# Kernel optimization log

Hardware: AMD Instinct MI355X
Metric: run time of the kernel (lower is better)

## Reference

```python
import jax, jax.numpy as jnp
import numpy as np

N, E, D, STEPS, MOLS, OUT = 50000, 400000, 128, 3, 256, 32


def setup_inputs() -> dict:
    key = jax.random.key(0)
    ks = jax.random.split(key, 20)
    s = 0.1  # weight scale ~ 1/sqrt(fan_in) to keep relu chain stable
    inp = {
        "states": jax.random.normal(ks[0], (N, D), jnp.float32),
        "Win": jax.random.normal(ks[1], (STEPS, 2 * D, 64), jnp.float32) * s,
        "b_in": jax.random.normal(ks[2], (STEPS, 64), jnp.float32) * s,
        "Wh": jax.random.normal(ks[3], (STEPS, 64, 64), jnp.float32) * s,
        "b_h": jax.random.normal(ks[4], (STEPS, 64), jnp.float32) * s,
        "Wout": jax.random.normal(ks[5], (STEPS, 64, D), jnp.float32) * s,
        "b_out": jax.random.normal(ks[6], (STEPS, D), jnp.float32) * s,
        "fc1_w": jax.random.normal(ks[7], (D, 64), jnp.float32) * s,
        "fc1_b": jax.random.normal(ks[8], (64,), jnp.float32) * s,
        "fc2_w": jax.random.normal(ks[9], (64, 64), jnp.float32) * s,
        "fc2_b": jax.random.normal(ks[10], (64,), jnp.float32) * s,
        "out_w": jax.random.normal(ks[11], (64, OUT), jnp.float32) * s,
        "out_b": jax.random.normal(ks[12], (OUT,), jnp.float32) * s,
        "src": jax.random.randint(ks[13], (E,), 0, N, jnp.int32).astype(jnp.int64),
        "dst": jax.random.randint(ks[14], (E,), 0, N, jnp.int32).astype(jnp.int64),
        "mol_ids": jax.random.randint(ks[15], (N,), 0, MOLS, jnp.int32).astype(jnp.int64),
        "num_mols": MOLS,
    }
    return inp


def reference(states, Win, b_in, Wh, b_h, Wout, b_out,
              fc1_w, fc1_b, fc2_w, fc2_b, out_w, out_b,
              src, dst, mol_ids, num_mols):
    n_atoms = states.shape[0]
    s = states
    for t in range(Win.shape[0]):  # message_steps (small, static)
        # per-edge message input: concat(owner state, neighbor state) -> [E, 2D]
        x = jnp.concatenate([s[dst], s[src]], axis=-1)
        m = jax.nn.relu(x @ Win[t] + b_in[t])
        m = jax.nn.relu(m @ Wh[t] + b_h[t])
        m = jax.nn.relu(m @ Wout[t] + b_out[t])  # [E, D]
        # atom-wise sum aggregation of incoming messages
        s = jax.ops.segment_sum(m, dst, num_segments=n_atoms)
    # molecule representation: sum of final atom states per molecule
    mol_repr = jax.ops.segment_sum(s, mol_ids, num_segments=num_mols)  # [M, D]
    h = jax.nn.relu(mol_repr @ fc1_w + fc1_b)
    h = jax.nn.relu(h @ fc2_w + fc2_b)
    return h @ out_w + out_b  # [M, OUT]
```

## Files before the change

kernel.cpp:

```cpp
#include <hip/hip_runtime.h>

typedef unsigned long long u64;
typedef unsigned short ushort_t;

#define NA 50000
#define NE 400000
#define DF 128
#define HID 64
#define NMOL 256
#define NOUT 32
#define NSTEP 3
#define NPB 782

#define RNG 8192
#define NRNG 7
#define NCH 64
#define CHUNK 6250
#define NCHM 16
#define CHM 3125
#define NWB 336
#define HISTB (NRNG*NCH + NCHM + NWB)
#define SCATB (NRNG*NCH + NCHM)
#define MBUF_ROWS 160000

typedef __attribute__((ext_vector_type(8))) unsigned short ushort8;
typedef __attribute__((ext_vector_type(4))) float f32x4;
typedef __attribute__((ext_vector_type(8))) _Float16 half8;
typedef __attribute__((ext_vector_type(2))) _Float16 half2_t;
typedef __attribute__((ext_vector_type(2))) __fp16 fp16x2;

static __device__ __forceinline__ ushort_t f2h(float f) {
  union { _Float16 h; ushort_t u; } v; v.h = (_Float16)f; return v.u;
}
static __device__ __forceinline__ float hlo(unsigned d) {
  union { unsigned u; half2_t h; } v; v.u = d; return (float)v.h[0];
}
static __device__ __forceinline__ float hhi(unsigned d) {
  union { unsigned u; half2_t h; } v; v.u = d; return (float)v.h[1];
}
static __device__ __forceinline__ unsigned pkrtz(float a, float b) {
  union { fp16x2 h; unsigned u; } v;
  v.h = __builtin_amdgcn_cvt_pkrtz(a, b);
  return v.u;
}

__global__ __launch_bounds__(256) void hist_all(
    const int* __restrict__ dst, const int* __restrict__ mol_ids,
    const float* __restrict__ Win, const float* __restrict__ Wh,
    const float* __restrict__ Wout,
    ushort_t* __restrict__ WpB, ushort_t* __restrict__ WhB,
    ushort_t* __restrict__ WoB,
    ushort_t* __restrict__ H, unsigned* __restrict__ MH,
    int* __restrict__ mcnt) {
  __shared__ unsigned hist[RNG];
  const int b = blockIdx.x, t = threadIdx.x;
  if (b < NRNG * NCH) {
    const int r = b / NCH, c = b % NCH;
    const int lo = r * RNG;
    for (int i = t; i < RNG; i += 256) hist[i] = 0;
    __syncthreads();
    const int base = c * CHUNK;
    for (int k = t; k < CHUNK; k += 256) {
      int d = dst[base + k];
      unsigned rel = (unsigned)(d - lo);
      if (rel < RNG) atomicAdd(&hist[rel], 1u);
    }
    __syncthreads();
    ushort_t* Hp = H + (u64)b * RNG;
    for (int i = t; i < RNG; i += 256) Hp[i] = (ushort_t)hist[i];
    return;
  }
  int b2 = b - NRNG * NCH;
  if (b2 < NCHM) {
    if (t < 256) hist[t] = 0;
    __syncthreads();
    const int base = b2 * CHM;
    for (int k = t; k < CHM; k += 256) atomicAdd(&hist[mol_ids[base + k]], 1u);
    __syncthreads();
    if (t < 256) {
      MH[b2 * 256 + t] = hist[t];
      if (hist[t]) atomicAdd(&mcnt[t], (int)hist[t]);
    }
    return;
  }
  int g = (b2 - NCHM) * 256 + t;
  if (g < 3 * 16384) {
    int tt = g / 16384, r = g % 16384;
    int j = r & 7, lane = (r >> 3) & 63, f = r >> 9;
    int kc = f & 3, nt = f >> 2;
    int k = kc * 32 + (lane >> 4) * 8 + j;
    int n = nt * 16 + (lane & 15);
    float v = (n < 64) ? Win[tt * 16384 + k * 64 + n]
                       : Win[tt * 16384 + (128 + k) * 64 + (n - 64)];
    WpB[g] = f2h(v);
  }
  int g2 = g - 3 * 16384;
  if (g2 >= 0 && g2 < 3 * 4096) {
    int tt = g2 / 4096, r = g2 % 4096;
    int j = r & 7, lane = (r >> 3) & 63, f = r >> 9;
    int kc = f & 1, nt = f >> 1;
    int k = kc * 32 + (lane >> 4) * 8 + j;
    int n = nt * 16 + (lane & 15);
    WhB[g2] = f2h(Wh[tt * 4096 + k * 64 + n]);
  }
  int g3 = g2 - 3 * 4096;
  if (g3 >= 0 && g3 < 3 * 8192) {
    int tt = g3 / 8192, r = g3 % 8192;
    int j = r & 7, lane = (r >> 3) & 63, f = r >> 9;
    int kc = f & 1, nt = f >> 1;
    int k = kc * 32 + (lane >> 4) * 8 + j;
    int n = nt * 16 + (lane & 15);
    WoB[g3] = f2h(Wout[tt * 8192 + k * 128 + n]);
  }
}

__global__ void col_scan(const ushort_t* __restrict__ H,
                         ushort_t* __restrict__ Orel, int* __restrict__ counts) {
  int bidx = blockIdx.x * 256 + threadIdx.x;
  if (bidx >= NA) return;
  int r = bidx >> 13, i = bidx & (RNG - 1);
  const ushort_t* Hp = H + ((u64)r * NCH) * RNG + i;
  unsigned acc = 0;
  for (int c = 0; c < NCH; c++) {
    Orel[(u64)c * NA + bidx] = (ushort_t)acc;
    acc += Hp[(u64)c * RNG];
  }
  counts[bidx] = (int)acc;
}

__global__ void scan_phase1(const int* __restrict__ counts, int* __restrict__ tmp,
                            int* __restrict__ blk,
                            const int* __restrict__ mcnt, int* __restrict__ mrow) {
  __shared__ int sh[1024];
  int t = threadIdx.x;
  int i = blockIdx.x * 1024 + t;
  sh[t] = (i < NA) ? counts[i] : 0;
  __syncthreads();
  for (int off = 1; off < 1024; off <<= 1) {
    int x = (t >= off) ? sh[t - off] : 0;
    __syncthreads();
    sh[t] += x;
    __syncthreads();
  }
  if (i < NA) tmp[i] = sh[t];
  if (t == 1023) blk[blockIdx.x] = sh[1023];
  if (blockIdx.x == gridDim.x - 1) {
    __syncthreads();
    sh[t] = (t < NMOL) ? mcnt[t] : 0;
    __syncthreads();
    for (int off = 1; off < NMOL; off <<= 1) {
      int x = (t >= off && t < NMOL) ? sh[t - off] : 0;
      __syncthreads();
      if (t < NMOL) sh[t] += x;
      __syncthreads();
    }
    if (t < NMOL) mrow[t + 1] = sh[t];
    if (t == 0) mrow[0] = 0;
  }
}

__global__ void scan_phase3(const int* __restrict__ tmp, const int* __restrict__ blk,
                            int* __restrict__ row_ptr,
                            int* __restrict__ ntmp, int* __restrict__ nblk) {
  __shared__ int sh[1024];
  __shared__ int spre_sh;
  int t = threadIdx.x;
  int bid = blockIdx.x;
  if (t < 64) {
    int v = (t < bid) ? blk[t] : 0;
    for (int off = 32; off; off >>= 1) v += __shfl_down(v, off);
    if (t == 0) spre_sh = v;
  }
  __syncthreads();
  int spre = spre_sh;
  int i = bid * 1024 + t;
  int nwin = 0;
  if (i < NA) {
    int re = tmp[i] + spre;
    int rs = (t == 0) ? spre : (tmp[i - 1] + spre);
    row_ptr[i + 1] = re;
    if (re > rs) nwin = ((re - 1) >> 2) - (rs >> 2) + 1;
  }
  if (i == 0) row_ptr[0] = 0;
  sh[t] = nwin;
  __syncthreads();
  for (int off = 1; off < 1024; off <<= 1) {
    int x = (t >= off) ? sh[t - off] : 0;
    __syncthreads();
    sh[t] += x;
    __syncthreads();
  }
  if (i < NA) ntmp[i] = sh[t];
  if (t == 1023) nblk[bid] = sh[1023];
}

__global__ void nscan_p3(const int* __restrict__ ntmp, const int* __restrict__ nblk,
                         const int* __restrict__ row_ptr,
                         int* __restrict__ orow, int* __restrict__ orow2) {
  __shared__ int spre_sh;
  int t = threadIdx.x;
  int bid = blockIdx.x;
  if (t < 64) {
    int v = (t < bid) ? nblk[t] : 0;
    for (int off = 32; off; off >>= 1) v += __shfl_down(v, off);
    if (t == 0) spre_sh = v;
  }
  __syncthreads();
  int spre = spre_sh;
  int i = bid * 1024 + t;
  if (i < NA) {
    orow[i + 1] = ntmp[i] + spre;
    int oi = (t == 0) ? spre : (ntmp[i - 1] + spre);
    orow2[i] = oi - (row_ptr[i] >> 2);
  }
  if (i == 0) orow[0] = 0;
}

__global__ __launch_bounds__(256) void scat_all(
    const int* __restrict__ dst, const int* __restrict__ src,
    const int* __restrict__ row_ptr, const ushort_t* __restrict__ Orel,
    unsigned* __restrict__ ds_pack,
    const int* __restrict__ mol_ids, const int* __restrict__ mrow,
    const unsigned* __restrict__ MH, int* __restrict__ mol_sorted) {
  __shared__ unsigned cnt[RNG];
  __shared__ unsigned mbase[256];
  const int b = blockIdx.x, t = threadIdx.x;
  if (b < NRNG * NCH) {
    const int r = b / NCH, c = b % NCH;
    const int lo = r * RNG;
    for (int i = t; i < RNG; i += 256) cnt[i] = 0;
    __syncthreads();
    const int base = c * CHUNK;
    const ushort_t* Op = Orel + (u64)c * NA;
    for (int k = t; k < CHUNK; k += 256) {
      int e = base + k;
      int d = dst[e];
      unsigned rel = (unsigned)(d - lo);
      if (rel < RNG) {
        unsigned lr = atomicAdd(&cnt[rel], 1u);
        int pos = row_ptr[d] + (int)Op[d] + (int)lr;
        ds_pack[pos] = ((unsigned)d << 16) | (unsigned)src[e];
      }
    }
    return;
  }
  const int c2 = b - NRNG * NCH;
  if (t < 256) {
    unsigned s = (unsigned)mrow[t];
    for (int cp = 0; cp < c2; cp++) s += MH[cp * 256 + t];
    mbase[t] = s;
    cnt[t] = 0;
  }
  __syncthreads();
  const int base = c2 * CHM;
  for (int k = t; k < CHM; k += 256) {
    int a = base + k;
    int m = mol_ids[a];
    unsigned lr = atomicAdd(&cnt[m], 1u);
    mol_sorted[mbase[m] + lr] = a;
  }
}

__global__ __launch_bounds__(256) void node_proj(
    const float* __restrict__ s_in, const ushort_t* __restrict__ WpB,
    const float* __restrict__ b_in, ushort_t* __restrict__ PQb) {
  const int t = threadIdx.x;
  const int lane = t & 63, wv = t >> 6, quad = lane >> 4, l15 = lane & 15;
  const int n0 = blockIdx.x * 64 + wv * 16;
  int n = n0 + l15; if (n >= NA) n = NA - 1;
  union { half8 v; unsigned d[4]; } a[4];
#pragma unroll
  for (int c = 0; c < 4; c++) {
    const float* p = s_in + (u64)n * 128 + c * 32 + quad * 8;
    float4 f0 = *(const float4*)(p);
    float4 f1 = *(const float4*)(p + 4);
    a[c].d[0] = pkrtz(f0.x, f0.y);
    a[c].d[1] = pkrtz(f0.z, f0.w);
    a[c].d[2] = pkrtz(f1.x, f1.y);
    a[c].d[3] = pkrtz(f1.z, f1.w);
  }
  float binv[4];
#pragma unroll
  for (int nt = 0; nt < 4; nt++) binv[nt] = b_in[nt * 16 + l15];
#pragma unroll
  for (int nt = 0; nt < 8; nt++) {
    f32x4 acc = {0.f, 0.f, 0.f, 0.f};
#pragma unroll
    for (int c = 0; c < 4; c++) {
      half8 b = *(const half8*)&WpB[((nt * 4 + c) * 64 + lane) * 8];
      acc = __builtin_amdgcn_mfma_f32_16x16x32_f16(a[c].v, b, acc, 0, 0, 0);
    }
    float bias = (nt < 4) ? binv[nt] : 0.f;
#pragma unroll
    for (int r = 0; r < 4; r++) {
      int nn = n0 + quad * 4 + r;
      if (nn < NA) PQb[(u64)nn * 128 + nt * 16 + l15] = f2h(acc[r] + bias);
    }
  }
}

__global__ __launch_bounds__(256) void edge_msg(
    const ushort_t* __restrict__ PQb,
    const ushort_t* __restrict__ WhB, const ushort_t* __restrict__ WoB,
    const float* __restrict__ b_h, const float* __restrict__ b_out,
    const unsigned* __restrict__ ds_pack, const int* __restrict__ orow2,
    unsigned* __restrict__ m_buf) {
  __shared__ unsigned eps[128];
  __shared__ int ops[128];
  __shared__ ushort_t h2s[4][16 * 72];
  const int t = threadIdx.x;
  const int lane = t & 63, wv = t >> 6, quad = lane >> 4, l15 = lane & 15;
  const long long e0 = (long long)blockIdx.x * 128;

  if (t < 128) {
    long long e = e0 + t;
    unsigned pk = ds_pack[e];
    eps[t] = pk;
    ops[t] = orow2[pk >> 16] + (int)(e >> 2);
  }
  float bh[4], bo[8];
#pragma unroll
  for (int nt = 0; nt < 4; nt++) bh[nt] = b_h[nt * 16 + l15];
#pragma unroll
  for (int nt = 0; nt < 8; nt++) bo[nt] = b_out[nt * 16 + l15];
  __syncthreads();

  union PQ { ushort8 v; half2_t h[4]; } pv[2][2], qv[2][2];
#pragma unroll
  for (int i = 0; i < 2; i++) {
    unsigned pk = eps[wv * 32 + i * 16 + l15];
    int da = pk >> 16, sa = pk & 0xffffu;
#pragma unroll
    for (int c = 0; c < 2; c++) {
      const int col = c * 32 + quad * 8;
      pv[i][c].v = *(const ushort8*)&PQb[(u64)da * 128 + col];
      qv[i][c].v = *(const ushort8*)&PQb[(u64)sa * 128 + 64 + col];
    }
  }

  const half2_t z2 = {(_Float16)0.f, (_Float16)0.f};
#pragma unroll
  for (int i = 0; i < 2; i++) {
    const int ebl = wv * 32 + i * 16;

    union { half8 v; half2_t h[4]; } a1[2];
#pragma unroll
    for (int c = 0; c < 2; c++) {
#pragma unroll
      for (int k = 0; k < 4; k++) {
        half2_t s = pv[i][c].h[k] + qv[i][c].h[k];
        a1[c].h[k] = __builtin_elementwise_max(s, z2);
      }
    }

    ushort_t* hb = h2s[wv];
#pragma unroll
    for (int nt = 0; nt < 4; nt++) {
      f32x4 acc = {0.f, 0.f, 0.f, 0.f};
#pragma unroll
      for (int c = 0; c < 2; c++) {
        half8 b = *(const half8*)&WhB[((nt * 2 + c) * 64 + lane) * 8];
        acc = __builtin_amdgcn_mfma_f32_16x16x32_f16(a1[c].v, b, acc, 0, 0, 0);
      }
#pragma unroll
      for (int r = 0; r < 4; r++)
        hb[(quad * 4 + r) * 72 + nt * 16 + l15] =
            f2h(fmaxf(acc[r] + bh[nt], 0.f));
    }

    half8 a2[2];
#pragma unroll
    for (int c = 0; c < 2; c++)
      a2[c] = *(const half8*)&hb[l15 * 72 + c * 32 + quad * 8];

    f32x4 acc2[8];
#pragma unroll
    for (int nt = 0; nt < 8; nt++) {
      f32x4 acc = {0.f, 0.f, 0.f, 0.f};
#pragma unroll
      for (int c = 0; c < 2; c++) {
        half8 b = *(const half8*)&WoB[((nt * 2 + c) * 64 + lane) * 8];
        acc = __builtin_amdgcn_mfma_f32_16x16x32_f16(a2[c], b, acc, 0, 0, 0);
      }
      acc2[nt] = acc;
    }

    {
      const int base = ebl + quad * 4;
      int prev = (int)(eps[base] >> 16);
      int orow_ = ops[base];
      float run[8];
#pragma unroll
      for (int nt = 0; nt < 8; nt++) run[nt] = 0.f;
#pragma unroll
      for (int r = 0; r < 4; r++) {
        int er = base + r;
        int dcur = (int)(eps[er] >> 16);
        if (dcur != prev) {
          unsigned* rowp = m_buf + (u64)orow_ * 64;
#pragma unroll
          for (int k = 0; k < 4; k++)
            rowp[k * 16 + l15] = pkrtz(run[2 * k], run[2 * k + 1]);
#pragma unroll
          for (int nt = 0; nt < 8; nt++) run[nt] = 0.f;
          prev = dcur; orow_ = ops[er];
        }
#pragma unroll
        for (int nt = 0; nt < 8; nt++)
          run[nt] += fmaxf(acc2[nt][r] + bo[nt], 0.f);
      }
      unsigned* rowp = m_buf + (u64)orow_ * 64;
#pragma unroll
      for (int k = 0; k < 4; k++)
        rowp[k * 16 + l15] = pkrtz(run[2 * k], run[2 * k + 1]);
    }
  }
}

__global__ __launch_bounds__(256) void agg_proj(
    const unsigned* __restrict__ m_buf, const int* __restrict__ orow,
    const ushort_t* __restrict__ WpB, const float* __restrict__ b_in,
    ushort_t* __restrict__ PQb) {
  __shared__ ushort_t a_s[64 * 136];
  __shared__ int obs_s[65];
  const int t = threadIdx.x;
  const int lane = t & 63, wv = t >> 6, quad = lane >> 4, l15 = lane & 15;
  const int n0 = blockIdx.x * 64;
  if (t < 65) {
    int idx = n0 + t; if (idx > NA) idx = NA;
    obs_s[t] = orow[idx];
  }
  __syncthreads();

  for (int r = 0; r < 16; r++) {
    const int d = n0 + wv * 16 + r;
    float s0 = 0.f, s1 = 0.f;
    if (d < NA) {
      int ob = obs_s[wv * 16 + r], oe = obs_s[wv * 16 + r + 1];
      int n = oe - ob;
      float t0 = 0.f, t1 = 0.f, u0 = 0.f, u1 = 0.f, v0 = 0.f, v1 = 0.f;
      int full = n & ~3;
      int e = ob;
      for (; e < ob + full; e += 4) {
        unsigned w0 = m_buf[(u64)(e + 0) * 64 + lane];
        unsigned w1 = m_buf[(u64)(e + 1) * 64 + lane];
        unsigned w2 = m_buf[(u64)(e + 2) * 64 + lane];
        unsigned w3 = m_buf[(u64)(e + 3) * 64 + lane];
        s0 += hlo(w0); s1 += hhi(w0);
        t0 += hlo(w1); t1 += hhi(w1);
        u0 += hlo(w2); u1 += hhi(w2);
        v0 += hlo(w3); v1 += hhi(w3);
      }
      int rem = n - full;
      if (rem > 0) {
        int i1 = (rem > 1) ? e + 1 : e;
        int i2 = (rem > 2) ? e + 2 : e;
        unsigned w0 = m_buf[(u64)e * 64 + lane];
        unsigned w1 = m_buf[(u64)i1 * 64 + lane];
        unsigned w2 = m_buf[(u64)i2 * 64 + lane];
        s0 += hlo(w0); s1 += hhi(w0);
        if (rem > 1) { t0 += hlo(w1); t1 += hhi(w1); }
        if (rem > 2) { u0 += hlo(w2); u1 += hhi(w2); }
      }
      s0 = (s0 + t0) + (u0 + v0);
      s1 = (s1 + t1) + (u1 + v1);
    }
    const int row = wv * 16 + r;
    a_s[row * 136 + quad * 32 + l15] = f2h(s0);
    a_s[row * 136 + quad * 32 + 16 + l15] = f2h(s1);
  }

  float binv[4];
#pragma unroll
  for (int nt = 0; nt < 4; nt++) binv[nt] = b_in[nt * 16 + l15];
  half8 a[4];
#pragma unroll
  for (int c = 0; c < 4; c++)
    a[c] = *(const half8*)&a_s[(wv * 16 + l15) * 136 + c * 32 + quad * 8];
#pragma unroll
  for (int nt = 0; nt < 8; nt++) {
    f32x4 acc = {0.f, 0.f, 0.f, 0.f};
#pragma unroll
    for (int c = 0; c < 4; c++) {
      half8 b = *(const half8*)&WpB[((nt * 4 + c) * 64 + lane) * 8];
      acc = __builtin_amdgcn_mfma_f32_16x16x32_f16(a[c], b, acc, 0, 0, 0);
    }
    float bias = (nt < 4) ? binv[nt] : 0.f;
#pragma unroll
    for (int r = 0; r < 4; r++) {
      int nn = n0 + wv * 16 + quad * 4 + r;
      if (nn < NA) PQb[(u64)nn * 128 + nt * 16 + l15] = f2h(acc[r] + bias);
    }
  }
}

__global__ __launch_bounds__(256) void agg_mol2(
    const unsigned* __restrict__ m_buf, const int* __restrict__ orow,
    const int* __restrict__ mol_sorted, const int* __restrict__ mol_ids,
    float* __restrict__ mol_repr) {
  __shared__ int mids[64], obs[64], oes[64];
  const int t = threadIdx.x;
  const int lane = t & 63, wv = t >> 6;
  const int base = blockIdx.x * 64;
  if (t < 64) {
    int idx = base + t;
    int r = (idx < NA) ? mol_sorted[idx] : 0;
    mids[t] = (idx < NA) ? mol_ids[r] : -1;
    obs[t] = orow[r];
    oes[t] = orow[r + 1];
  }
  __syncthreads();
  const int c0 = (lane >> 4) * 32 + (lane & 15);
  float r0 = 0.f, r1 = 0.f;
  int prev = mids[wv * 16];
  for (int i = 0; i < 16; i++) {
    int li = wv * 16 + i;
    int m = mids[li];
    if (m != prev) {
      if (prev >= 0) {
        atomicAdd(&mol_repr[(u64)prev * 128 + c0], r0);
        atomicAdd(&mol_repr[(u64)prev * 128 + c0 + 16], r1);
      }
      r0 = 0.f; r1 = 0.f; prev = m;
    }
    if (m >= 0) {
      int ob = obs[li], oe = oes[li];
      int n = oe - ob;
      float t0 = 0.f, t1 = 0.f, u0 = 0.f, u1 = 0.f, v0 = 0.f, v1 = 0.f;
      int full = n & ~3;
      int e = ob;
      for (; e < ob + full; e += 4) {
        unsigned w0 = m_buf[(u64)(e + 0) * 64 + lane];
        unsigned w1 = m_buf[(u64)(e + 1) * 64 + lane];
        unsigned w2 = m_buf[(u64)(e + 2) * 64 + lane];
        unsigned w3 = m_buf[(u64)(e + 3) * 64 + lane];
        r0 += hlo(w0); r1 += hhi(w0);
        t0 += hlo(w1); t1 += hhi(w1);
        u0 += hlo(w2); u1 += hhi(w2);
        v0 += hlo(w3); v1 += hhi(w3);
      }
      int rem = n - full;
      if (rem > 0) {
        int i1 = (rem > 1) ? e + 1 : e;
        int i2 = (rem > 2) ? e + 2 : e;
        unsigned w0 = m_buf[(u64)e * 64 + lane];
        unsigned w1 = m_buf[(u64)i1 * 64 + lane];
        unsigned w2 = m_buf[(u64)i2 * 64 + lane];
        r0 += hlo(w0); r1 += hhi(w0);
        if (rem > 1) { t0 += hlo(w1); t1 += hhi(w1); }
        if (rem > 2) { u0 += hlo(w2); u1 += hhi(w2); }
      }
      r0 += (t0 + u0) + v0;
      r1 += (t1 + u1) + v1;
    }
  }
  if (prev >= 0) {
    atomicAdd(&mol_repr[(u64)prev * 128 + c0], r0);
    atomicAdd(&mol_repr[(u64)prev * 128 + c0 + 16], r1);
  }
}

__global__ void final_mlp(const float* __restrict__ mol_repr,
                          const float* __restrict__ fc1_w, const float* __restrict__ fc1_b,
                          const float* __restrict__ fc2_w, const float* __restrict__ fc2_b,
                          const float* __restrict__ out_w, const float* __restrict__ out_b,
                          float* __restrict__ out) {
  int m = blockIdx.x, j = threadIdx.x;
  __shared__ float h1sh[64], h2sh[64];
  const float* mr = mol_repr + (u64)m * DF;
  float acc = fc1_b[j];
  for (int d = 0; d < DF; d++) acc = fmaf(mr[d], fc1_w[d * 64 + j], acc);
  h1sh[j] = fmaxf(acc, 0.f);
  __syncthreads();
  acc = fc2_b[j];
  for (int k = 0; k < 64; k++) acc = fmaf(h1sh[k], fc2_w[k * 64 + j], acc);
  h2sh[j] = fmaxf(acc, 0.f);
  __syncthreads();
  if (j < NOUT) {
    acc = out_b[j];
    for (int k = 0; k < 64; k++) acc = fmaf(h2sh[k], out_w[k * NOUT + j], acc);
    out[(u64)m * NOUT + j] = acc;
  }
}

extern "C" void kernel_launch(void* const* d_in, const int* in_sizes, int n_in,
                              void* d_out, int out_size, void* d_ws, size_t ws_size,
                              hipStream_t stream) {
  const float* states = (const float*)d_in[0];
  const float* Win    = (const float*)d_in[1];
  const float* b_in   = (const float*)d_in[2];
  const float* Wh     = (const float*)d_in[3];
  const float* b_h    = (const float*)d_in[4];
  const float* Wout   = (const float*)d_in[5];
  const float* b_out  = (const float*)d_in[6];
  const float* fc1_w  = (const float*)d_in[7];
  const float* fc1_b  = (const float*)d_in[8];
  const float* fc2_w  = (const float*)d_in[9];
  const float* fc2_b  = (const float*)d_in[10];
  const float* out_w  = (const float*)d_in[11];
  const float* out_b  = (const float*)d_in[12];
  const int* src      = (const int*)d_in[13];
  const int* dst      = (const int*)d_in[14];
  const int* mol_ids  = (const int*)d_in[15];

  char* ws = (char*)d_ws;
  u64 o = 0;
  auto alloc = [&](u64 bytes) {
    void* p = ws + o;
    o += (bytes + 255) & ~255ull;
    return p;
  };
  unsigned* m_buf = (unsigned*)alloc((u64)MBUF_ROWS * 64 * 4);
  ushort_t* PQb  = (ushort_t*)alloc((u64)NA * DF * 2);
  ushort_t* WpB  = (ushort_t*)alloc(3 * 16384 * 2);
  ushort_t* WhB  = (ushort_t*)alloc(3 * 4096 * 2);
  ushort_t* WoB  = (ushort_t*)alloc(3 * 8192 * 2);
  char* zbase    = ws + o;
  float* molr    = (float*)alloc((u64)NMOL * DF * 4);
  int* mcnt      = (int*)alloc(NMOL * 4);
  u64 zbytes     = (u64)((ws + o) - zbase);
  int* counts    = (int*)alloc((u64)NA * 4);
  int* row_ptr   = (int*)alloc((u64)(NA + 1) * 4);
  int* mrow      = (int*)alloc((NMOL + 1) * 4);
  unsigned* ds_pack = (unsigned*)alloc((u64)NE * 4);
  int* mol_sorted = (int*)alloc((u64)NA * 4);
  int* scan_tmp  = (int*)alloc((u64)NA * 4);
  int* blk_sums  = (int*)alloc(64 * 4);
  int* ntmp      = (int*)alloc((u64)NA * 4);
  int* nblk      = (int*)alloc(64 * 4);
  int* orow      = (int*)alloc((u64)(NA + 1) * 4);
  int* orow2     = (int*)alloc((u64)NA * 4);
  ushort_t* H    = (ushort_t*)alloc((u64)NRNG * NCH * RNG * 2);
  ushort_t* Orel = (ushort_t*)alloc((u64)NCH * NA * 2);
  unsigned* MH   = (unsigned*)alloc((u64)NCHM * 256 * 4);
  (void)ws_size; (void)in_sizes; (void)n_in; (void)out_size;

  const int NSCAN = (NA + 1023) / 1024;

  hipMemsetAsync(zbase, 0, zbytes, stream);

  hist_all<<<HISTB, 256, 0, stream>>>(dst, mol_ids, Win, Wh, Wout,
                                      WpB, WhB, WoB, H, MH, mcnt);
  col_scan<<<(NA + 255) / 256, 256, 0, stream>>>(H, Orel, counts);
  scan_phase1<<<NSCAN, 1024, 0, stream>>>(counts, scan_tmp, blk_sums, mcnt, mrow);
  scan_phase3<<<NSCAN, 1024, 0, stream>>>(scan_tmp, blk_sums, row_ptr, ntmp, nblk);
  nscan_p3<<<NSCAN, 1024, 0, stream>>>(ntmp, nblk, row_ptr, orow, orow2);
  scat_all<<<SCATB, 256, 0, stream>>>(dst, src, row_ptr, Orel, ds_pack,
                                      mol_ids, mrow, MH, mol_sorted);

  node_proj<<<NPB, 256, 0, stream>>>(states, WpB, b_in, PQb);
  for (int t = 0; t < NSTEP; t++) {
    edge_msg<<<(NE + 127) / 128, 256, 0, stream>>>(
        PQb, WhB + t * 4096, WoB + t * 8192,
        b_h + t * 64, b_out + t * 128, ds_pack, orow2, m_buf);
    if (t < NSTEP - 1) {
      agg_proj<<<(NA + 63) / 64, 256, 0, stream>>>(m_buf, orow,
                                                   WpB + (t + 1) * 16384,
                                                   b_in + (t + 1) * 64, PQb);
    } else {
      agg_mol2<<<(NA + 63) / 64, 256, 0, stream>>>(m_buf, orow, mol_sorted,
                                                   mol_ids, molr);
    }
  }
  final_mlp<<<NMOL, 64, 0, stream>>>(molr, fc1_w, fc1_b, fc2_w, fc2_b, out_w, out_b,
                                     (float*)d_out);
}
```

Measured before the change: 306.6 us.

## Fuse edge messages, aggregation and next projection into one node-tiled kernel

Replaces the per-step edge_msg + agg_proj/agg_mol2 pair with a single kernel where each block owns 64 destination nodes, processes their dst-sorted edge range, and accumulates messages into an LDS float buffer via shared atomics before applying the next step's projection. This removes the m_buf round trip through global memory, the window-offset scans (ntmp/orow/orow2), and several launches, and adds double-buffered gathers of the PQ rows. It risks load imbalance since blocks now get variable edge counts, adds LDS atomic contention and a large shared buffer that lowers occupancy, and needs ping-pong PQ buffers plus an fp32 s_final array for the last step.

```diff
diff --git a/kernel.cpp b/kernel.cpp
--- a/kernel.cpp
+++ b/kernel.cpp
@@ -21,7 +21,6 @@
 #define NWB 336
 #define HISTB (NRNG*NCH + NCHM + NWB)
 #define SCATB (NRNG*NCH + NCHM)
-#define MBUF_ROWS 160000
 
 typedef __attribute__((ext_vector_type(8))) unsigned short ushort8;
 typedef __attribute__((ext_vector_type(4))) float f32x4;
@@ -31,12 +30,6 @@
 
 static __device__ __forceinline__ ushort_t f2h(float f) {
   union { _Float16 h; ushort_t u; } v; v.h = (_Float16)f; return v.u;
-}
-static __device__ __forceinline__ float hlo(unsigned d) {
-  union { unsigned u; half2_t h; } v; v.u = d; return (float)v.h[0];
-}
-static __device__ __forceinline__ float hhi(unsigned d) {
-  union { unsigned u; half2_t h; } v; v.u = d; return (float)v.h[1];
 }
 static __device__ __forceinline__ unsigned pkrtz(float a, float b) {
   union { fp16x2 h; unsigned u; } v;
@@ -160,9 +153,7 @@
 }
 
 __global__ void scan_phase3(const int* __restrict__ tmp, const int* __restrict__ blk,
-                            int* __restrict__ row_ptr,
-                            int* __restrict__ ntmp, int* __restrict__ nblk) {
-  __shared__ int sh[1024];
+                            int* __restrict__ row_ptr) {
   __shared__ int spre_sh;
   int t = threadIdx.x;
   int bid = blockIdx.x;
@@ -174,46 +165,8 @@
   __syncthreads();
   int spre = spre_sh;
   int i = bid * 1024 + t;
-  int nwin = 0;
-  if (i < NA) {
-    int re = tmp[i] + spre;
-    int rs = (t == 0) ? spre : (tmp[i - 1] + spre);
-    row_ptr[i + 1] = re;
-    if (re > rs) nwin = ((re - 1) >> 2) - (rs >> 2) + 1;
-  }
+  if (i < NA) row_ptr[i + 1] = tmp[i] + spre;
   if (i == 0) row_ptr[0] = 0;
-  sh[t] = nwin;
-  __syncthreads();
-  for (int off = 1; off < 1024; off <<= 1) {
-    int x = (t >= off) ? sh[t - off] : 0;
-    __syncthreads();
-    sh[t] += x;
-    __syncthreads();
-  }
-  if (i < NA) ntmp[i] = sh[t];
-  if (t == 1023) nblk[bid] = sh[1023];
-}
-
-__global__ void nscan_p3(const int* __restrict__ ntmp, const int* __restrict__ nblk,
-                         const int* __restrict__ row_ptr,
-                         int* __restrict__ orow, int* __restrict__ orow2) {
-  __shared__ int spre_sh;
-  int t = threadIdx.x;
-  int bid = blockIdx.x;
-  if (t < 64) {
-    int v = (t < bid) ? nblk[t] : 0;
-    for (int off = 32; off; off >>= 1) v += __shfl_down(v, off);
-    if (t == 0) spre_sh = v;
-  }
-  __syncthreads();
-  int spre = spre_sh;
-  int i = bid * 1024 + t;
-  if (i < NA) {
-    orow[i + 1] = ntmp[i] + spre;
-    int oi = (t == 0) ? spre : (ntmp[i - 1] + spre);
-    orow2[i] = oi - (row_ptr[i] >> 2);
-  }
-  if (i == 0) orow[0] = 0;
 }
 
 __global__ __launch_bounds__(256) void scat_all(
@@ -299,25 +252,26 @@
   }
 }
 
-__global__ __launch_bounds__(256) void edge_msg(
+template <bool LAST>
+__global__ __launch_bounds__(256) void edge_fused(
     const ushort_t* __restrict__ PQb,
     const ushort_t* __restrict__ WhB, const ushort_t* __restrict__ WoB,
     const float* __restrict__ b_h, const float* __restrict__ b_out,
-    const unsigned* __restrict__ ds_pack, const int* __restrict__ orow2,
-    unsigned* __restrict__ m_buf) {
-  __shared__ unsigned eps[128];
-  __shared__ int ops[128];
+    const unsigned* __restrict__ ds_pack, const int* __restrict__ row_ptr,
+    const ushort_t* __restrict__ WpB, const float* __restrict__ b_in,
+    ushort_t* __restrict__ PQo, float* __restrict__ s_final) {
+  __shared__ float s_acc[64][132];
   __shared__ ushort_t h2s[4][16 * 72];
   const int t = threadIdx.x;
   const int lane = t & 63, wv = t >> 6, quad = lane >> 4, l15 = lane & 15;
-  const long long e0 = (long long)blockIdx.x * 128;
-
-  if (t < 128) {
-    long long e = e0 + t;
-    unsigned pk = ds_pack[e];
-    eps[t] = pk;
-    ops[t] = orow2[pk >> 16] + (int)(e >> 2);
-  }
+  const int n0 = blockIdx.x * 64;
+  {
+    float* p = &s_acc[0][0];
+    for (int i = t; i < 64 * 132; i += 256) p[i] = 0.f;
+  }
+  const int rb = row_ptr[n0];
+  const int re = row_ptr[(n0 + 64 < NA) ? (n0 + 64) : NA];
+
   float bh[4], bo[8];
 #pragma unroll
   for (int nt = 0; nt < 4; nt++) bh[nt] = b_h[nt * 16 + l15];
@@ -325,180 +279,177 @@
   for (int nt = 0; nt < 8; nt++) bo[nt] = b_out[nt * 16 + l15];
   __syncthreads();
 
-  union PQ { ushort8 v; half2_t h[4]; } pv[2][2], qv[2][2];
-#pragma unroll
-  for (int i = 0; i < 2; i++) {
-    unsigned pk = eps[wv * 32 + i * 16 + l15];
-    int da = pk >> 16, sa = pk & 0xffffu;
-#pragma unroll
-    for (int c = 0; c < 2; c++) {
-      const int col = c * 32 + quad * 8;
-      pv[i][c].v = *(const ushort8*)&PQb[(u64)da * 128 + col];
-      qv[i][c].v = *(const ushort8*)&PQb[(u64)sa * 128 + 64 + col];
-    }
-  }
+  struct GB {
+    unsigned pk0, pk1;
+    ushort8 p0c0, p0c1, p1c0, p1c1;
+    ushort8 q0c0, q0c1, q1c0, q1c1;
+  };
+
+  const int colq = quad * 8;
+  auto load_g = [&](GB& b, int g) {
+    int e0 = g + l15;       if (e0 > re - 1) e0 = re - 1;
+    int e1 = g + 16 + l15;  if (e1 > re - 1) e1 = re - 1;
+    unsigned k0 = ds_pack[e0], k1 = ds_pack[e1];
+    b.pk0 = k0; b.pk1 = k1;
+    {
+      u64 da = k0 >> 16, sa = k0 & 0xffffu;
+      b.p0c0 = *(const ushort8*)&PQb[da * 128 + colq];
+      b.p0c1 = *(const ushort8*)&PQb[da * 128 + 32 + colq];
+      b.q0c0 = *(const ushort8*)&PQb[sa * 128 + 64 + colq];
+      b.q0c1 = *(const ushort8*)&PQb[sa * 128 + 96 + colq];
+    }
+    {
+      u64 da = k1 >> 16, sa = k1 & 0xffffu;
+      b.p1c0 = *(const ushort8*)&PQb[da * 128 + colq];
+      b.p1c1 = *(const ushort8*)&PQb[da * 128 + 32 + colq];
+      b.q1c0 = *(const ushort8*)&PQb[sa * 128 + 64 + colq];
+      b.q1c1 = *(const ushort8*)&PQb[sa * 128 + 96 + colq];
+    }
+  };
 
   const half2_t z2 = {(_Float16)0.f, (_Float16)0.f};
-#pragma unroll
-  for (int i = 0; i < 2; i++) {
-    const int ebl = wv * 32 + i * 16;
-
-    union { half8 v; half2_t h[4]; } a1[2];
-#pragma unroll
-    for (int c = 0; c < 2; c++) {
-#pragma unroll
-      for (int k = 0; k < 4; k++) {
-        half2_t s = pv[i][c].h[k] + qv[i][c].h[k];
-        a1[c].h[k] = __builtin_elementwise_max(s, z2);
-      }
-    }
-
+  auto do_tile = [&](ushort8 pc0, ushort8 pc1, ushort8 qc0, ushort8 qc1,
+                     unsigned pk, int tb) {
+    union UPQ { ushort8 u; half2_t h[4]; };
+    UPQ P0, P1, Q0, Q1;
+    P0.u = pc0; P1.u = pc1; Q0.u = qc0; Q1.u = qc1;
+    union { half8 v; half2_t h[4]; } a1c0, a1c1;
+#pragma unroll
+    for (int k = 0; k < 4; k++) {
+      half2_t s0 = P0.h[k] + Q0.h[k];
+      half2_t s1 = P1.h[k] + Q1.h[k];
+      a1c0.h[k] = __builtin_elementwise_max(s0, z2);
+      a1c1.h[k] = __builtin_elementwise_max(s1, z2);
+    }
     ushort_t* hb = h2s[wv];
 #pragma unroll
     for (int nt = 0; nt < 4; nt++) {
       f32x4 acc = {0.f, 0.f, 0.f, 0.f};
-#pragma unroll
-      for (int c = 0; c < 2; c++) {
-        half8 b = *(const half8*)&WhB[((nt * 2 + c) * 64 + lane) * 8];
-        acc = __builtin_amdgcn_mfma_f32_16x16x32_f16(a1[c].v, b, acc, 0, 0, 0);
-      }
+      half8 b0 = *(const half8*)&WhB[((nt * 2 + 0) * 64 + lane) * 8];
+      acc = __builtin_amdgcn_mfma_f32_16x16x32_f16(a1c0.v, b0, acc, 0, 0, 0);
+      half8 b1 = *(const half8*)&WhB[((nt * 2 + 1) * 64 + lane) * 8];
+      acc = __builtin_amdgcn_mfma_f32_16x16x32_f16(a1c1.v, b1, acc, 0, 0, 0);
 #pragma unroll
       for (int r = 0; r < 4; r++)
         hb[(quad * 4 + r) * 72 + nt * 16 + l15] =
             f2h(fmaxf(acc[r] + bh[nt], 0.f));
     }
-
-    half8 a2[2];
-#pragma unroll
-    for (int c = 0; c < 2; c++)
-      a2[c] = *(const half8*)&hb[l15 * 72 + c * 32 + quad * 8];
-
+    half8 a2c0 = *(const half8*)&hb[l15 * 72 + quad * 8];
+    half8 a2c1 = *(const half8*)&hb[l15 * 72 + 32 + quad * 8];
     f32x4 acc2[8];
 #pragma unroll
     for (int nt = 0; nt < 8; nt++) {
       f32x4 acc = {0.f, 0.f, 0.f, 0.f};
-#pragma unroll
-      for (int c = 0; c < 2; c++) {
-        half8 b = *(const half8*)&WoB[((nt * 2 + c) * 64 + lane) * 8];
-        acc = __builtin_amdgcn_mfma_f32_16x16x32_f16(a2[c], b, acc, 0, 0, 0);
-      }
+      half8 b0 = *(const half8*)&WoB[((nt * 2 + 0) * 64 + lane) * 8];
+      acc = __builtin_amdgcn_mfma_f32_16x16x32_f16(a2c0, b0, acc, 0, 0, 0);
+      half8 b1 = *(const half8*)&WoB[((nt * 2 + 1) * 64 + lane) * 8];
+      acc = __builtin_amdgcn_mfma_f32_16x16x32_f16(a2c1, b1, acc, 0, 0, 0);
       acc2[nt] = acc;
     }
-
-    {
-      const int base = ebl + quad * 4;
-      int prev = (int)(eps[base] >> 16);
-      int orow_ = ops[base];
-      float run[8];
-#pragma unroll
-      for (int nt = 0; nt < 8; nt++) run[nt] = 0.f;
-#pragma unroll
-      for (int r = 0; r < 4; r++) {
-        int er = base + r;
-        int dcur = (int)(eps[er] >> 16);
-        if (dcur != prev) {
-          unsigned* rowp = m_buf + (u64)orow_ * 64;
-#pragma unroll
-          for (int k = 0; k < 4; k++)
-            rowp[k * 16 + l15] = pkrtz(run[2 * k], run[2 * k + 1]);
-#pragma unroll
-          for (int nt = 0; nt < 8; nt++) run[nt] = 0.f;
-          prev = dcur; orow_ = ops[er];
-        }
+    int pks[4];
+#pragma unroll
+    for (int r = 0; r < 4; r++)
+      pks[r] = __shfl((int)pk, (lane & 48) + quad * 4 + r);
+    unsigned prev = ((unsigned)pks[0]) >> 16;
+    float run[8];
+#pragma unroll
+    for (int nt = 0; nt < 8; nt++) run[nt] = 0.f;
+#pragma unroll
+    for (int r = 0; r < 4; r++) {
+      unsigned dcur = ((unsigned)pks[r]) >> 16;
+      int er = tb + quad * 4 + r;
+      if (dcur != prev) {
+        int dl = (int)prev - n0;
+#pragma unroll
+        for (int nt = 0; nt < 8; nt++)
+          atomicAdd(&s_acc[dl][nt * 16 + l15], run[nt]);
+#pragma unroll
+        for (int nt = 0; nt < 8; nt++) run[nt] = 0.f;
+        prev = dcur;
+      }
+      if (er < re) {
 #pragma unroll
         for (int nt = 0; nt < 8; nt++)
           run[nt] += fmaxf(acc2[nt][r] + bo[nt], 0.f);
       }
-      unsigned* rowp = m_buf + (u64)orow_ * 64;
-#pragma unroll
-      for (int k = 0; k < 4; k++)
-        rowp[k * 16 + l15] = pkrtz(run[2 * k], run[2 * k + 1]);
-    }
-  }
-}
-
-__global__ __launch_bounds__(256) void agg_proj(
-    const unsigned* __restrict__ m_buf, const int* __restrict__ orow,
-    const ushort_t* __restrict__ WpB, const float* __restrict__ b_in,
-    ushort_t* __restrict__ PQb) {
-  __shared__ ushort_t a_s[64 * 136];
-  __shared__ int obs_s[65];
-  const int t = threadIdx.x;
-  const int lane = t & 63, wv = t >> 6, quad = lane >> 4, l15 = lane & 15;
-  const int n0 = blockIdx.x * 64;
-  if (t < 65) {
-    int idx = n0 + t; if (idx > NA) idx = NA;
-    obs_s[t] = orow[idx];
-  }
-  __syncthreads();
-
-  for (int r = 0; r < 16; r++) {
-    const int d = n0 + wv * 16 + r;
-    float s0 = 0.f, s1 = 0.f;
-    if (d < NA) {
-      int ob = obs_s[wv * 16 + r], oe = obs_s[wv * 16 + r + 1];
-      int n = oe - ob;
-      float t0 = 0.f, t1 = 0.f, u0 = 0.f, u1 = 0.f, v0 = 0.f, v1 = 0.f;
-      int full = n & ~3;
-      int e = ob;
-      for (; e < ob + full; e += 4) {
-        unsigned w0 = m_buf[(u64)(e + 0) * 64 + lane];
-        unsigned w1 = m_buf[(u64)(e + 1) * 64 + lane];
-        unsigned w2 = m_buf[(u64)(e + 2) * 64 + lane];
-        unsigned w3 = m_buf[(u64)(e + 3) * 64 + lane];
-        s0 += hlo(w0); s1 += hhi(w0);
-        t0 += hlo(w1); t1 += hhi(w1);
-        u0 += hlo(w2); u1 += hhi(w2);
-        v0 += hlo(w3); v1 += hhi(w3);
-      }
-      int rem = n - full;
-      if (rem > 0) {
-        int i1 = (rem > 1) ? e + 1 : e;
-        int i2 = (rem > 2) ? e + 2 : e;
-        unsigned w0 = m_buf[(u64)e * 64 + lane];
-        unsigned w1 = m_buf[(u64)i1 * 64 + lane];
-        unsigned w2 = m_buf[(u64)i2 * 64 + lane];
-        s0 += hlo(w0); s1 += hhi(w0);
-        if (rem > 1) { t0 += hlo(w1); t1 += hhi(w1); }
-        if (rem > 2) { u0 += hlo(w2); u1 += hhi(w2); }
-      }
-      s0 = (s0 + t0) + (u0 + v0);
-      s1 = (s1 + t1) + (u1 + v1);
-    }
-    const int row = wv * 16 + r;
-    a_s[row * 136 + quad * 32 + l15] = f2h(s0);
-    a_s[row * 136 + quad * 32 + 16 + l15] = f2h(s1);
-  }
-
-  float binv[4];
-#pragma unroll
-  for (int nt = 0; nt < 4; nt++) binv[nt] = b_in[nt * 16 + l15];
-  half8 a[4];
-#pragma unroll
-  for (int c = 0; c < 4; c++)
-    a[c] = *(const half8*)&a_s[(wv * 16 + l15) * 136 + c * 32 + quad * 8];
-#pragma unroll
-  for (int nt = 0; nt < 8; nt++) {
-    f32x4 acc = {0.f, 0.f, 0.f, 0.f};
+    }
+    {
+      int dl = (int)prev - n0;
+#pragma unroll
+      for (int nt = 0; nt < 8; nt++)
+        atomicAdd(&s_acc[dl][nt * 16 + l15], run[nt]);
+    }
+  };
+
+  int g = rb + wv * 32;
+  GB bA, bB;
+  if (g < re) load_g(bA, g);
+  while (g < re) {
+    int g1 = g + 128;
+    if (g1 < re) load_g(bB, g1);
+    do_tile(bA.p0c0, bA.p0c1, bA.q0c0, bA.q0c1, bA.pk0, g);
+    do_tile(bA.p1c0, bA.p1c1, bA.q1c0, bA.q1c1, bA.pk1, g + 16);
+    g = g1;
+    if (g >= re) break;
+    int g2 = g + 128;
+    if (g2 < re) load_g(bA, g2);
+    do_tile(bB.p0c0, bB.p0c1, bB.q0c0, bB.q0c1, bB.pk0, g);
+    do_tile(bB.p1c0, bB.p1c1, bB.q1c0, bB.q1c1, bB.pk1, g + 16);
+    g = g2;
+  }
+  __syncthreads();
+
+  if (!LAST) {
+    float binv[4];
+#pragma unroll
+    for (int nt = 0; nt < 4; nt++) binv[nt] = b_in[nt * 16 + l15];
+    const int row = wv * 16 + l15;
+    half8 a[4];
 #pragma unroll
     for (int c = 0; c < 4; c++) {
-      half8 b = *(const half8*)&WpB[((nt * 4 + c) * 64 + lane) * 8];
-      acc = __builtin_amdgcn_mfma_f32_16x16x32_f16(a[c], b, acc, 0, 0, 0);
-    }
-    float bias = (nt < 4) ? binv[nt] : 0.f;
-#pragma unroll
-    for (int r = 0; r < 4; r++) {
-      int nn = n0 + wv * 16 + quad * 4 + r;
-      if (nn < NA) PQb[(u64)nn * 128 + nt * 16 + l15] = f2h(acc[r] + bias);
-    }
-  }
-}
-
-__global__ __launch_bounds__(256) void agg_mol2(
-    const unsigned* __restrict__ m_buf, const int* __restrict__ orow,
-    const int* __restrict__ mol_sorted, const int* __restrict__ mol_ids,
-    float* __restrict__ mol_repr) {
-  __shared__ int mids[64], obs[64], oes[64];
+      f32x4 lo = *(const f32x4*)&s_acc[row][c * 32 + quad * 8];
+      f32x4 hi = *(const f32x4*)&s_acc[row][c * 32 + quad * 8 + 4];
+      union { half8 v; unsigned d[4]; } av;
+      av.d[0] = pkrtz(lo[0], lo[1]);
+      av.d[1] = pkrtz(lo[2], lo[3]);
+      av.d[2] = pkrtz(hi[0], hi[1]);
+      av.d[3] = pkrtz(hi[2], hi[3]);
+      a[c] = av.v;
+    }
+#pragma unroll
+    for (int nt = 0; nt < 8; nt++) {
+      f32x4 acc = {0.f, 0.f, 0.f, 0.f};
+#pragma unroll
+      for (int c = 0; c < 4; c++) {
+        half8 b = *(const half8*)&WpB[((nt * 4 + c) * 64 + lane) * 8];
+        acc = __builtin_amdgcn_mfma_f32_16x16x32_f16(a[c], b, acc, 0, 0, 0);
+      }
+      float bias = (nt < 4) ? binv[nt] : 0.f;
+#pragma unroll
+      for (int r = 0; r < 4; r++) {
+        int nn = n0 + wv * 16 + quad * 4 + r;
+        if (nn < NA) PQo[(u64)nn * 128 + nt * 16 + l15] = f2h(acc[r] + bias);
+      }
+    }
+  } else {
+    const int row = wv * 16 + l15;
+    const int nn = n0 + row;
+    if (nn < NA) {
+#pragma unroll
+      for (int c = 0; c < 4; c++) {
+        *(float4*)&s_final[(u64)nn * 128 + c * 32 + quad * 8] =
+            *(const float4*)&s_acc[row][c * 32 + quad * 8];
+        *(float4*)&s_final[(u64)nn * 128 + c * 32 + quad * 8 + 4] =
+            *(const float4*)&s_acc[row][c * 32 + quad * 8 + 4];
+      }
+    }
+  }
+}
+
+__global__ __launch_bounds__(256) void agg_mol3(
+    const float* __restrict__ s_final, const int* __restrict__ mol_sorted,
+    const int* __restrict__ mol_ids, float* __restrict__ mol_repr) {
+  __shared__ int mids[64], rows[64];
   const int t = threadIdx.x;
   const int lane = t & 63, wv = t >> 6;
   const int base = blockIdx.x * 64;
@@ -506,8 +457,7 @@
     int idx = base + t;
     int r = (idx < NA) ? mol_sorted[idx] : 0;
     mids[t] = (idx < NA) ? mol_ids[r] : -1;
-    obs[t] = orow[r];
-    oes[t] = orow[r + 1];
+    rows[t] = r;
   }
   __syncthreads();
   const int c0 = (lane >> 4) * 32 + (lane & 15);
@@ -524,34 +474,9 @@
       r0 = 0.f; r1 = 0.f; prev = m;
     }
     if (m >= 0) {
-      int ob = obs[li], oe = oes[li];
-      int n = oe - ob;
-      float t0 = 0.f, t1 = 0.f, u0 = 0.f, u1 = 0.f, v0 = 0.f, v1 = 0.f;
-      int full = n & ~3;
-      int e = ob;
-      for (; e < ob + full; e += 4) {
-        unsigned w0 = m_buf[(u64)(e + 0) * 64 + lane];
-        unsigned w1 = m_buf[(u64)(e + 1) * 64 + lane];
-        unsigned w2 = m_buf[(u64)(e + 2) * 64 + lane];
-        unsigned w3 = m_buf[(u64)(e + 3) * 64 + lane];
-        r0 += hlo(w0); r1 += hhi(w0);
-        t0 += hlo(w1); t1 += hhi(w1);
-        u0 += hlo(w2); u1 += hhi(w2);
-        v0 += hlo(w3); v1 += hhi(w3);
-      }
-      int rem = n - full;
-      if (rem > 0) {
-        int i1 = (rem > 1) ? e + 1 : e;
-        int i2 = (rem > 2) ? e + 2 : e;
-        unsigned w0 = m_buf[(u64)e * 64 + lane];
-        unsigned w1 = m_buf[(u64)i1 * 64 + lane];
-        unsigned w2 = m_buf[(u64)i2 * 64 + lane];
-        r0 += hlo(w0); r1 += hhi(w0);
-        if (rem > 1) { t0 += hlo(w1); t1 += hhi(w1); }
-        if (rem > 2) { u0 += hlo(w2); u1 += hhi(w2); }
-      }
-      r0 += (t0 + u0) + v0;
-      r1 += (t1 + u1) + v1;
+      const float* rp = s_final + (u64)rows[li] * 128;
+      r0 += rp[c0];
+      r1 += rp[c0 + 16];
     }
   }
   if (prev >= 0) {
@@ -610,8 +535,9 @@
     o += (bytes + 255) & ~255ull;
     return p;
   };
-  unsigned* m_buf = (unsigned*)alloc((u64)MBUF_ROWS * 64 * 4);
-  ushort_t* PQb  = (ushort_t*)alloc((u64)NA * DF * 2);
+  ushort_t* PQa  = (ushort_t*)alloc((u64)NA * DF * 2);
+  ushort_t* PQc  = (ushort_t*)alloc((u64)NA * DF * 2);
+  float* s_final = (float*)alloc((u64)NA * DF * 4);
   ushort_t* WpB  = (ushort_t*)alloc(3 * 16384 * 2);
   ushort_t* WhB  = (ushort_t*)alloc(3 * 4096 * 2);
   ushort_t* WoB  = (ushort_t*)alloc(3 * 8192 * 2);
@@ -626,10 +552,6 @@
   int* mol_sorted = (int*)alloc((u64)NA * 4);
   int* scan_tmp  = (int*)alloc((u64)NA * 4);
   int* blk_sums  = (int*)alloc(64 * 4);
-  int* ntmp      = (int*)alloc((u64)NA * 4);
-  int* nblk      = (int*)alloc(64 * 4);
-  int* orow      = (int*)alloc((u64)(NA + 1) * 4);
-  int* orow2     = (int*)alloc((u64)NA * 4);
   ushort_t* H    = (ushort_t*)alloc((u64)NRNG * NCH * RNG * 2);
   ushort_t* Orel = (ushort_t*)alloc((u64)NCH * NA * 2);
   unsigned* MH   = (unsigned*)alloc((u64)NCHM * 256 * 4);
@@ -643,25 +565,21 @@
                                       WpB, WhB, WoB, H, MH, mcnt);
   col_scan<<<(NA + 255) / 256, 256, 0, stream>>>(H, Orel, counts);
   scan_phase1<<<NSCAN, 1024, 0, stream>>>(counts, scan_tmp, blk_sums, mcnt, mrow);
-  scan_phase3<<<NSCAN, 1024, 0, stream>>>(scan_tmp, blk_sums, row_ptr, ntmp, nblk);
-  nscan_p3<<<NSCAN, 1024, 0, stream>>>(ntmp, nblk, row_ptr, orow, orow2);
+  scan_phase3<<<NSCAN, 1024, 0, stream>>>(scan_tmp, blk_sums, row_ptr);
   scat_all<<<SCATB, 256, 0, stream>>>(dst, src, row_ptr, Orel, ds_pack,
                                       mol_ids, mrow, MH, mol_sorted);
 
-  node_proj<<<NPB, 256, 0, stream>>>(states, WpB, b_in, PQb);
-  for (int t = 0; t < NSTEP; t++) {
-    edge_msg<<<(NE + 127) / 128, 256, 0, stream>>>(
-        PQb, WhB + t * 4096, WoB + t * 8192,
-        b_h + t * 64, b_out + t * 128, ds_pack, orow2, m_buf);
-    if (t < NSTEP - 1) {
-      agg_proj<<<(NA + 63) / 64, 256, 0, stream>>>(m_buf, orow,
-                                                   WpB + (t + 1) * 16384,
-                                                   b_in + (t + 1) * 64, PQb);
-    } else {
-      agg_mol2<<<(NA + 63) / 64, 256, 0, stream>>>(m_buf, orow, mol_sorted,
-                                                   mol_ids, molr);
-    }
-  }
+  node_proj<<<NPB, 256, 0, stream>>>(states, WpB, b_in, PQa);
+  edge_fused<false><<<NPB, 256, 0, stream>>>(
+      PQa, WhB + 0 * 4096, WoB + 0 * 8192, b_h + 0 * 64, b_out + 0 * 128,
+      ds_pack, row_ptr, WpB + 1 * 16384, b_in + 1 * 64, PQc, s_final);
+  edge_fused<false><<<NPB, 256, 0, stream>>>(
+      PQc, WhB + 1 * 4096, WoB + 1 * 8192, b_h + 1 * 64, b_out + 1 * 128,
+      ds_pack, row_ptr, WpB + 2 * 16384, b_in + 2 * 64, PQa, s_final);
+  edge_fused<true><<<NPB, 256, 0, stream>>>(
+      PQa, WhB + 2 * 4096, WoB + 2 * 8192, b_h + 2 * 64, b_out + 2 * 128,
+      ds_pack, row_ptr, WpB, b_in, PQc, s_final);
+  agg_mol3<<<(NA + 63) / 64, 256, 0, stream>>>(s_final, mol_sorted, mol_ids, molr);
   final_mlp<<<NMOL, 64, 0, stream>>>(molr, fc1_w, fc1_b, fc2_w, fc2_b, out_w, out_b,
                                      (float*)d_out);
 }
```

Measured after the change: 684.6 us. 2.23x slower.
